# Kernel tuning notes

Measured on AMD Instinct MI355X. Metric: run time of the kernel, lower is better.

## Reference

```python
import jax, jax.numpy as jnp
import numpy as np

C = 256
HEADS = 4
GROUPS = 8
EPS = 1e-5


def setup_inputs() -> dict:
    key = jax.random.key(0)
    ks = jax.random.split(key, 7)
    B, H, W = 2, 64, 64
    x = jax.random.normal(ks[0], (B, C, H, W), dtype=jnp.float32)
    gamma = jnp.ones((C,), dtype=jnp.float32)
    beta = jnp.zeros((C,), dtype=jnp.float32)
    # conv 1x1 weights stored as [out_ch, in_ch]
    w_qkv = jax.random.normal(ks[1], (3 * C, C), dtype=jnp.float32) * (1.0 / np.sqrt(C))
    b_qkv = jax.random.normal(ks[2], (3 * C,), dtype=jnp.float32) * 0.01
    w_proj = jax.random.normal(ks[3], (C, C), dtype=jnp.float32) * (1.0 / np.sqrt(C))
    b_proj = jax.random.normal(ks[4], (C,), dtype=jnp.float32) * 0.01
    return {"x": x, "gamma": gamma, "beta": beta, "w_qkv": w_qkv,
            "b_qkv": b_qkv, "w_proj": w_proj, "b_proj": b_proj}


def _group_norm(x, gamma, beta):
    B, Cc, H, W = x.shape
    xg = x.reshape(B, GROUPS, Cc // GROUPS, H, W)
    mean = xg.mean(axis=(2, 3, 4), keepdims=True)
    var = xg.var(axis=(2, 3, 4), keepdims=True)
    xg = (xg - mean) * jax.lax.rsqrt(var + EPS)
    xn = xg.reshape(B, Cc, H, W)
    return xn * gamma[None, :, None, None] + beta[None, :, None, None]


def reference(x, gamma, beta, w_qkv, b_qkv, w_proj, b_proj):
    B, Cc, H, W = x.shape
    N = H * W
    hd = Cc // HEADS
    residual = x
    xn = _group_norm(x, gamma, beta)
    # 1x1 conv == channel matmul: [B,3C,H,W]
    qkv = jnp.einsum('oc,bchw->bohw', w_qkv, xn) + b_qkv[None, :, None, None]
    # [B,3,heads,hd,N] -> (3,B,heads,N,hd)
    qkv = qkv.reshape(B, 3, HEADS, hd, N).transpose(1, 0, 2, 4, 3)
    q, k, v = qkv[0], qkv[1], qkv[2]
    scale = hd ** -0.5
    attn = jax.nn.softmax(jnp.einsum('bhnd,bhmd->bhnm', q, k) * scale, axis=-1)
    out = jnp.einsum('bhnm,bhmd->bhnd', attn, v)  # [B,heads,N,hd]
    out = out.transpose(0, 1, 3, 2).reshape(B, Cc, H, W)
    out = jnp.einsum('oc,bchw->bohw', w_proj, out) + b_proj[None, :, None, None]
    return out + residual
```

## Files before the change

### kernel.cpp

```cpp
#include <hip/hip_runtime.h>
#include <stdint.h>

#define EPS 1e-5f

typedef float f32x4 __attribute__((ext_vector_type(4)));
typedef float f32x16 __attribute__((ext_vector_type(16)));
typedef __bf16 bf16x8 __attribute__((ext_vector_type(8)));
typedef uint32_t u32x4 __attribute__((ext_vector_type(4)));

__device__ __forceinline__ ushort f2bf(float f){
  union { float f; uint32_t u; } v; v.f = f;
  uint32_t r = v.u + 0x7fffu + ((v.u >> 16) & 1u);
  return (ushort)(r >> 16);
}

__device__ __forceinline__ float bf2f(ushort u){
  union { uint32_t u; float f; } v; v.u = ((uint32_t)u) << 16;
  return v.f;
}

__device__ __forceinline__ uint32_t pk2bf(float a, float b){
  __bf16 x = (__bf16)a, y = (__bf16)b;
  return (uint32_t)__builtin_bit_cast(ushort, x) |
         ((uint32_t)__builtin_bit_cast(ushort, y) << 16);
}

__device__ __forceinline__ f32x4 mfma16(bf16x8 a, bf16x8 b, f32x4 c){
  return __builtin_amdgcn_mfma_f32_16x16x32_bf16(a, b, c, 0, 0, 0);
}
__device__ __forceinline__ f32x16 mfma32(bf16x8 a, bf16x8 b, f32x16 c){
  return __builtin_amdgcn_mfma_f32_32x32x16_bf16(a, b, c, 0, 0, 0);
}

__global__ __launch_bounds__(256) void k_pg(const float* wq, const float* wp, const float* x,
                                            ushort* wqb, ushort* wpb, float2* part){
  __shared__ float red[8];
  int bid = blockIdx.x;
  if (bid < 768){
    int i = bid * 256 + threadIdx.x;
    if (i < 3*256*256) wqb[i] = f2bf(wq[i]);
    if (i < 256*256)   wpb[i] = f2bf(wp[i]);
    return;
  }
  int gb = bid - 768;
  int bg = gb >> 6, pb = gb & 63;
  const f32x4* base = (const f32x4*)(x + (size_t)bg*131072 + (size_t)pb*2048);
  float s = 0.f, ss = 0.f;
  #pragma unroll
  for (int it = 0; it < 2; ++it){
    f32x4 v = base[threadIdx.x + it*256];
    #pragma unroll
    for (int j = 0; j < 4; ++j){ s += v[j]; ss += v[j]*v[j]; }
  }
  #pragma unroll
  for (int off = 1; off < 64; off <<= 1){
    s  += __shfl_xor(s,  off);
    ss += __shfl_xor(ss, off);
  }
  int wid = threadIdx.x >> 6;
  if ((threadIdx.x & 63) == 0){ red[wid] = s; red[4 + wid] = ss; }
  __syncthreads();
  if (threadIdx.x == 0){
    part[gb] = make_float2(red[0]+red[1]+red[2]+red[3],
                           red[4]+red[5]+red[6]+red[7]);
  }
}

__global__ __launch_bounds__(512) void k_nqkv(const float* x, const float* gamma, const float* beta,
                                              const float2* part, const ushort* wqb, const float* bqkv,
                                              ushort* Qb, ushort* Kb, ushort* Vb){
  __shared__ ushort A[32][264];
  __shared__ ushort Cl[32][136];
  __shared__ float2 st[8];
  int nt = blockIdx.x, b = blockIdx.y;
  int t = threadIdx.x, lane = t & 63, wid = t >> 6;

  {
    float2 p = part[(b*8 + wid)*64 + lane];
    float s = p.x, ss = p.y;
    #pragma unroll
    for (int off = 1; off < 64; off <<= 1){
      s  += __shfl_xor(s,  off);
      ss += __shfl_xor(ss, off);
    }
    if (lane == 0){
      const float inv = 1.f / 131072.f;
      float mean = s * inv;
      float var  = ss * inv - mean*mean;
      st[wid] = make_float2(mean, rsqrtf(var + EPS));
    }
  }
  __syncthreads();

  {
    int c = t >> 1, nh = t & 1;
    float2 s0 = st[c >> 5];
    float g  = gamma[c] * s0.y;
    float bt = beta[c] - s0.x * g;
    const float* xr = x + ((size_t)(b*256 + c))*4096 + nt*32 + nh*16;
    #pragma unroll
    for (int j4 = 0; j4 < 4; ++j4){
      f32x4 v = *(const f32x4*)(xr + j4*4);
      #pragma unroll
      for (int e = 0; e < 4; ++e) A[nh*16 + j4*4 + e][c] = f2bf(v[e]*g + bt);
    }
  }
  __syncthreads();

  int l15 = lane & 15, g4 = lane >> 4;
  f32x4 acc[6][2];
  #pragma unroll
  for (int of = 0; of < 6; ++of)
    #pragma unroll
    for (int mf = 0; mf < 2; ++mf) acc[of][mf] = (f32x4){0.f,0.f,0.f,0.f};

  #pragma unroll
  for (int ks = 0; ks < 8; ++ks){
    bf16x8 a0 = *(const bf16x8*)&A[l15][ks*32 + g4*8];
    bf16x8 a1 = *(const bf16x8*)&A[16 + l15][ks*32 + g4*8];
    #pragma unroll
    for (int of = 0; of < 6; ++of){
      int o = of*128 + wid*16 + l15;
      bf16x8 bw = *(const bf16x8*)(wqb + (size_t)o*256 + ks*32 + g4*8);
      acc[of][0] = mfma16(a0, bw, acc[of][0]);
      acc[of][1] = mfma16(a1, bw, acc[of][1]);
    }
  }

  #pragma unroll
  for (int of = 0; of < 6; ++of){
    __syncthreads();
    int o = of*128 + wid*16 + l15;
    float bias = bqkv[o];
    #pragma unroll
    for (int mf = 0; mf < 2; ++mf)
      #pragma unroll
      for (int r = 0; r < 4; ++r)
        Cl[mf*16 + g4*4 + r][wid*16 + l15] = f2bf(acc[of][mf][r] + bias);
    __syncthreads();
    if (of < 4){
      ushort* basep = (of < 2) ? Qb : Kb;
      int nl = t >> 4, oc = (t & 15) * 8;
      int h = (of & 1)*2 + (oc >> 6), d0 = oc & 63;
      ushort* dst = basep + (((size_t)(b*4 + h))*4096 + nt*32 + nl)*64 + d0;
      *(uint4*)dst = *(uint4*)&Cl[nl][oc];
    } else {
      int dl = t >> 2, nc = (t & 3) * 8;
      int h = (of - 4)*2 + (dl >> 6), d = dl & 63;
      uint32_t pk[4];
      #pragma unroll
      for (int j = 0; j < 4; ++j){
        uint32_t lo = Cl[nc + 2*j][dl], hiu = Cl[nc + 2*j + 1][dl];
        pk[j] = lo | (hiu << 16);
      }
      ushort* dst = Vb + (((size_t)(b*4 + h))*64 + d)*4096 + nt*32 + nc;
      *(uint4*)dst = make_uint4(pk[0], pk[1], pk[2], pk[3]);
    }
  }
}

template<int SPLIT>
__global__ __launch_bounds__(256, 2) void k_attn(const ushort* Qb, const ushort* Kb,
                                                 const ushort* Vb, ushort* Opart, float2* ML){
  const float SCL2 = 0.125f * 1.44269504f;
  const int per_xcd = 16 * SPLIT;
  int xb = (blockIdx.x & 7) * per_xcd + (blockIdx.x >> 3);
  int bh = xb / per_xcd;
  int within = xb % per_xcd;
  int sp = within >> 4, q4 = within & 15;
  int t = threadIdx.x, wid = t >> 6, l = t & 63, l31 = l & 31, hi = l >> 5;
  int qt = q4*4 + wid;

  const ushort* Qg = Qb + (size_t)bh*262144;
  const ushort* Kg = Kb + (size_t)bh*262144;
  const ushort* Vg = Vb + (size_t)bh*262144;

  bf16x8 qf[2][4];
  #pragma unroll
  for (int q2 = 0; q2 < 2; ++q2)
    #pragma unroll
    for (int dsub = 0; dsub < 4; ++dsub)
      qf[q2][dsub] = *(const bf16x8*)(Qg + (size_t)(qt*64 + q2*32 + l31)*64 + dsub*16 + hi*8);

  int rowp = (l31 & 19) | ((l31 & 4) << 1) | ((l31 & 8) >> 1);
  const ushort* Kbase = Kg + (size_t)rowp*64 + hi*8;
  const ushort* Vbase = Vg + (size_t)l31*4096 + hi*8;

  f32x16 o[2][2];
  #pragma unroll
  for (int dt = 0; dt < 2; ++dt)
    #pragma unroll
    for (int q2 = 0; q2 < 2; ++q2)
      #pragma unroll
      for (int r = 0; r < 16; ++r) o[dt][q2][r] = 0.f;
  float m_s[2] = {-INFINITY, -INFINITY};
  float l_s[2] = {0.f, 0.f};

  const int kbBeg = sp * (64 / SPLIT), kbEnd = kbBeg + 64 / SPLIT;
  for (int kb = kbBeg; kb < kbEnd; ++kb){
    bf16x8 kf[2][4];
    #pragma unroll
    for (int kt = 0; kt < 2; ++kt)
      #pragma unroll
      for (int dsub = 0; dsub < 4; ++dsub)
        kf[kt][dsub] = *(const bf16x8*)(Kbase + (size_t)(kb*64 + kt*32)*64 + dsub*16);

    f32x16 s[2][2];
    __builtin_amdgcn_s_setprio(1);
    #pragma unroll
    for (int kt = 0; kt < 2; ++kt)
      #pragma unroll
      for (int q2 = 0; q2 < 2; ++q2){
        f32x16 acc;
        #pragma unroll
        for (int r = 0; r < 16; ++r) acc[r] = 0.f;
        #pragma unroll
        for (int dsub = 0; dsub < 4; ++dsub)
          acc = mfma32(kf[kt][dsub], qf[q2][dsub], acc);
        s[kt][q2] = acc;
      }
    __builtin_amdgcn_s_setprio(0);

    float vm[2];
    #pragma unroll
    for (int q2 = 0; q2 < 2; ++q2){
      float v = s[0][q2][0];
      #pragma unroll
      for (int kt = 0; kt < 2; ++kt)
        #pragma unroll
        for (int r = 0; r < 16; ++r) v = fmaxf(v, s[kt][q2][r]);
      v = fmaxf(v, __shfl_xor(v, 32));
      vm[q2] = v * SCL2;
    }
    if (__any(fmaxf(vm[0] - m_s[0], vm[1] - m_s[1]) > 8.f)){
      #pragma unroll
      for (int q2 = 0; q2 < 2; ++q2){
        float mn = fmaxf(m_s[q2], vm[q2]);
        float a = __builtin_amdgcn_exp2f(m_s[q2] - mn);
        m_s[q2] = mn; l_s[q2] *= a;
        #pragma unroll
        for (int dt = 0; dt < 2; ++dt)
          #pragma unroll
          for (int r = 0; r < 16; ++r) o[dt][q2][r] *= a;
      }
    }
    #pragma unroll
    for (int q2 = 0; q2 < 2; ++q2){
      float r0 = 0.f, r1 = 0.f, r2 = 0.f, r3 = 0.f;
      #pragma unroll
      for (int kt = 0; kt < 2; ++kt)
        #pragma unroll
        for (int r = 0; r < 16; r += 4){
          float e0 = __builtin_amdgcn_exp2f(__builtin_fmaf(s[kt][q2][r+0], SCL2, -m_s[q2]));
          float e1 = __builtin_amdgcn_exp2f(__builtin_fmaf(s[kt][q2][r+1], SCL2, -m_s[q2]));
          float e2 = __builtin_amdgcn_exp2f(__builtin_fmaf(s[kt][q2][r+2], SCL2, -m_s[q2]));
          float e3 = __builtin_amdgcn_exp2f(__builtin_fmaf(s[kt][q2][r+3], SCL2, -m_s[q2]));
          s[kt][q2][r+0] = e0; s[kt][q2][r+1] = e1;
          s[kt][q2][r+2] = e2; s[kt][q2][r+3] = e3;
          r0 += e0; r1 += e1; r2 += e2; r3 += e3;
        }
      float rr = (r0 + r1) + (r2 + r3);
      rr += __shfl_xor(rr, 32);
      l_s[q2] += rr;
    }

    bf16x8 pf[2][2][2];
    #pragma unroll
    for (int kt = 0; kt < 2; ++kt)
      #pragma unroll
      for (int ks = 0; ks < 2; ++ks)
        #pragma unroll
        for (int q2 = 0; q2 < 2; ++q2){
          u32x4 w;
          #pragma unroll
          for (int c = 0; c < 4; ++c)
            w[c] = pk2bf(s[kt][q2][8*ks + 2*c], s[kt][q2][8*ks + 2*c + 1]);
          pf[kt][ks][q2] = __builtin_bit_cast(bf16x8, w);
        }

    bf16x8 vf[2][4];
    #pragma unroll
    for (int dt = 0; dt < 2; ++dt)
      #pragma unroll
      for (int c4 = 0; c4 < 4; ++c4)
        vf[dt][c4] = *(const bf16x8*)(Vbase + (size_t)dt*131072 + kb*64 + c4*16);

    __builtin_amdgcn_s_setprio(1);
    #pragma unroll
    for (int dt = 0; dt < 2; ++dt)
      #pragma unroll
      for (int q2 = 0; q2 < 2; ++q2)
        #pragma unroll
        for (int kt = 0; kt < 2; ++kt)
          #pragma unroll
          for (int ks = 0; ks < 2; ++ks)
            o[dt][q2] = mfma32(vf[dt][kt*2 + ks], pf[kt][ks][q2], o[dt][q2]);
    __builtin_amdgcn_s_setprio(0);
  }

  int pw = (bh*SPLIT + sp)*64 + qt;
  if (hi == 0){
    ML[(size_t)pw*64 + l31]      = make_float2(m_s[0], l_s[0]);
    ML[(size_t)pw*64 + 32 + l31] = make_float2(m_s[1], l_s[1]);
  }
  ushort* dst = Opart + (size_t)pw*4096;
  #pragma unroll
  for (int q2 = 0; q2 < 2; ++q2){
    int nl = q2*32 + l31;
    #pragma unroll
    for (int dt = 0; dt < 2; ++dt)
      #pragma unroll
      for (int rq = 0; rq < 4; ++rq){
        int d0 = dt*32 + rq*8 + 4*hi;
        uint2 w = make_uint2(pk2bf(o[dt][q2][rq*4+0], o[dt][q2][rq*4+1]),
                             pk2bf(o[dt][q2][rq*4+2], o[dt][q2][rq*4+3]));
        *(uint2*)(dst + (size_t)nl*64 + d0) = w;
      }
  }
}

template<int SPLIT>
__global__ __launch_bounds__(256) void k_comb(const ushort* Opart, const float2* ML, ushort* AO){
  int qt = blockIdx.x, bh = blockIdx.y;
  int b = bh >> 2, h = bh & 3;
  int t = threadIdx.x, ql = t >> 2, d0 = (t & 3) * 16;

  float2 mls[SPLIT];
  float m = -INFINITY;
  #pragma unroll
  for (int sp = 0; sp < SPLIT; ++sp){
    mls[sp] = ML[((size_t)((bh*SPLIT + sp)*64 + qt))*64 + ql];
    m = fmaxf(m, mls[sp].x);
  }
  float den = 0.f, w[SPLIT];
  #pragma unroll
  for (int sp = 0; sp < SPLIT; ++sp){
    w[sp] = __builtin_amdgcn_exp2f(mls[sp].x - m);
    den += mls[sp].y * w[sp];
  }
  float inv = 1.f / den;

  float vals[16];
  #pragma unroll
  for (int j = 0; j < 16; ++j) vals[j] = 0.f;
  #pragma unroll
  for (int sp = 0; sp < SPLIT; ++sp){
    const ushort* src = Opart + ((size_t)((bh*SPLIT + sp)*64 + qt))*4096 + (size_t)ql*64 + d0;
    uint4 a0 = *(const uint4*)src;
    uint4 a1 = *(const uint4*)(src + 8);
    float f = w[sp] * inv;
    #pragma unroll
    for (int j = 0; j < 8; ++j) vals[j]   += bf2f(((const ushort*)&a0)[j]) * f;
    #pragma unroll
    for (int j = 0; j < 8; ++j) vals[j+8] += bf2f(((const ushort*)&a1)[j]) * f;
  }
  uint32_t pk[8];
  #pragma unroll
  for (int j = 0; j < 8; ++j) pk[j] = pk2bf(vals[2*j], vals[2*j+1]);
  ushort* dst = AO + ((size_t)b*4096 + qt*64 + ql)*256 + h*64 + d0;
  *(uint4*)dst       = make_uint4(pk[0], pk[1], pk[2], pk[3]);
  *(uint4*)(dst + 8) = make_uint4(pk[4], pk[5], pk[6], pk[7]);
}

__global__ __launch_bounds__(256) void k_proj(const ushort* AO, const ushort* wpb, const float* bproj,
                                              const float* x, float* out){
  int nt = blockIdx.x, ct = blockIdx.y, b = blockIdx.z;
  int t = threadIdx.x, lane = t & 63, wid = t >> 6, l15 = lane & 15, g4 = lane >> 4;
  int o = ct*64 + wid*16 + l15;
  f32x4 acc[4];
  #pragma unroll
  for (int m = 0; m < 4; ++m) acc[m] = (f32x4){0.f,0.f,0.f,0.f};

  #pragma unroll
  for (int ks = 0; ks < 8; ++ks){
    bf16x8 bw = *(const bf16x8*)(wpb + (size_t)o*256 + ks*32 + g4*8);
    #pragma unroll
    for (int mf = 0; mf < 4; ++mf){
      int n = nt*64 + mf*16 + l15;
      bf16x8 aa = *(const bf16x8*)(AO + ((size_t)b*4096 + n)*256 + ks*32 + g4*8);
      acc[mf] = mfma16(aa, bw, acc[mf]);
    }
  }

  float bias = bproj[o];
  size_t cbase = ((size_t)b*256 + o)*4096;
  #pragma unroll
  for (int mf = 0; mf < 4; ++mf){
    int n0 = nt*64 + mf*16 + g4*4;
    f32x4 res = *(const f32x4*)(x + cbase + n0);
    f32x4 ov;
    #pragma unroll
    for (int r = 0; r < 4; ++r) ov[r] = acc[mf][r] + bias + res[r];
    *(f32x4*)(out + cbase + n0) = ov;
  }
}

extern "C" void kernel_launch(void* const* d_in, const int* in_sizes, int n_in,
                              void* d_out, int out_size, void* d_ws, size_t ws_size,
                              hipStream_t stream) {
  const float* x     = (const float*)d_in[0];
  const float* gamma = (const float*)d_in[1];
  const float* beta  = (const float*)d_in[2];
  const float* wqkv  = (const float*)d_in[3];
  const float* bqkv  = (const float*)d_in[4];
  const float* wproj = (const float*)d_in[5];
  const float* bproj = (const float*)d_in[6];
  float* out = (float*)d_out;

  const size_t MiB = 1024*1024;
  char* ws = (char*)d_ws;
  float2* part   = (float2*)(ws + 0);
  ushort* wq_b   = (ushort*)(ws + 16384);
  ushort* wp_b   = (ushort*)(ws + 409600);
  ushort* Qb     = (ushort*)(ws + 1*MiB);
  ushort* Kb     = (ushort*)(ws + 5*MiB);
  ushort* Vb     = (ushort*)(ws + 9*MiB);
  ushort* AO     = (ushort*)(ws + 13*MiB);
  ushort* Opart  = (ushort*)(ws + 17*MiB);

  int split = (ws_size >= 35*MiB) ? 4 : (ws_size >= 26*MiB ? 2 : 1);
  float2* ML = (float2*)(ws + (17 + 4*(size_t)split)*MiB);

  k_pg  <<<1792, 256, 0, stream>>>(wqkv, wproj, x, wq_b, wp_b, part);
  k_nqkv<<<dim3(128,2), 512, 0, stream>>>(x, gamma, beta, part, wq_b, bqkv, Qb, Kb, Vb);
  if (split == 4){
    k_attn<4><<<512, 256, 0, stream>>>(Qb, Kb, Vb, Opart, ML);
    k_comb<4><<<dim3(64,8), 256, 0, stream>>>(Opart, ML, AO);
  } else if (split == 2){
    k_attn<2><<<256, 256, 0, stream>>>(Qb, Kb, Vb, Opart, ML);
    k_comb<2><<<dim3(64,8), 256, 0, stream>>>(Opart, ML, AO);
  } else {
    k_attn<1><<<128, 256, 0, stream>>>(Qb, Kb, Vb, Opart, ML);
    k_comb<1><<<dim3(64,8), 256, 0, stream>>>(Opart, ML, AO);
  }
  k_proj<<<dim3(64,4,2), 256, 0, stream>>>(AO, wp_b, bproj, x, out);
}
```

Measured before the change: 174.3 us.

## Shrink attention query tile per wave and fuse split-combine into projection

Each attention wave now handles 32 queries instead of 64. This halves the accumulator registers, lets the kernel request 4 blocks per CU, and doubles the grid. The V loads are issued before the QK MFMAs to overlap latency, and the XCD block swizzle is replaced with a plain bh-major mapping. The separate combine and projection kernels are merged into one kernel that combines the split partials into shared memory and then runs the output projection, so the AO round-trip and one launch go away. The trade-off is less reuse of each K/V load per wave, and the split=1 fallback is gone.

```diff
diff --git a/kernel.cpp b/kernel.cpp
--- a/kernel.cpp
+++ b/kernel.cpp
@@ -160,41 +160,34 @@
 }
 
 template<int SPLIT>
-__global__ __launch_bounds__(256, 2) void k_attn(const ushort* Qb, const ushort* Kb,
+__global__ __launch_bounds__(256, 4) void k_attn(const ushort* Qb, const ushort* Kb,
                                                  const ushort* Vb, ushort* Opart, float2* ML){
   const float SCL2 = 0.125f * 1.44269504f;
-  const int per_xcd = 16 * SPLIT;
-  int xb = (blockIdx.x & 7) * per_xcd + (blockIdx.x >> 3);
-  int bh = xb / per_xcd;
-  int within = xb % per_xcd;
-  int sp = within >> 4, q4 = within & 15;
+  int bh = blockIdx.x & 7;
+  int within = blockIdx.x >> 3;
+  int sp = within >> 5, qb = within & 31;
   int t = threadIdx.x, wid = t >> 6, l = t & 63, l31 = l & 31, hi = l >> 5;
-  int qt = q4*4 + wid;
+  int qt = qb*4 + wid;
 
   const ushort* Qg = Qb + (size_t)bh*262144;
   const ushort* Kg = Kb + (size_t)bh*262144;
   const ushort* Vg = Vb + (size_t)bh*262144;
 
-  bf16x8 qf[2][4];
-  #pragma unroll
-  for (int q2 = 0; q2 < 2; ++q2)
-    #pragma unroll
-    for (int dsub = 0; dsub < 4; ++dsub)
-      qf[q2][dsub] = *(const bf16x8*)(Qg + (size_t)(qt*64 + q2*32 + l31)*64 + dsub*16 + hi*8);
+  bf16x8 qf[4];
+  #pragma unroll
+  for (int dsub = 0; dsub < 4; ++dsub)
+    qf[dsub] = *(const bf16x8*)(Qg + (size_t)(qt*32 + l31)*64 + dsub*16 + hi*8);
 
   int rowp = (l31 & 19) | ((l31 & 4) << 1) | ((l31 & 8) >> 1);
   const ushort* Kbase = Kg + (size_t)rowp*64 + hi*8;
   const ushort* Vbase = Vg + (size_t)l31*4096 + hi*8;
 
-  f32x16 o[2][2];
+  f32x16 o[2];
   #pragma unroll
   for (int dt = 0; dt < 2; ++dt)
     #pragma unroll
-    for (int q2 = 0; q2 < 2; ++q2)
-      #pragma unroll
-      for (int r = 0; r < 16; ++r) o[dt][q2][r] = 0.f;
-  float m_s[2] = {-INFINITY, -INFINITY};
-  float l_s[2] = {0.f, 0.f};
+    for (int r = 0; r < 16; ++r) o[dt][r] = 0.f;
+  float m_s = -INFINITY, l_s = 0.f;
 
   const int kbBeg = sp * (64 / SPLIT), kbEnd = kbBeg + 64 / SPLIT;
   for (int kb = kbBeg; kb < kbEnd; ++kb){
@@ -205,193 +198,184 @@
       for (int dsub = 0; dsub < 4; ++dsub)
         kf[kt][dsub] = *(const bf16x8*)(Kbase + (size_t)(kb*64 + kt*32)*64 + dsub*16);
 
-    f32x16 s[2][2];
+    bf16x8 vf[2][4];
+    #pragma unroll
+    for (int dt = 0; dt < 2; ++dt)
+      #pragma unroll
+      for (int c4 = 0; c4 < 4; ++c4)
+        vf[dt][c4] = *(const bf16x8*)(Vbase + (size_t)dt*131072 + kb*64 + c4*16);
+
+    f32x16 s[2];
     __builtin_amdgcn_s_setprio(1);
     #pragma unroll
-    for (int kt = 0; kt < 2; ++kt)
-      #pragma unroll
-      for (int q2 = 0; q2 < 2; ++q2){
-        f32x16 acc;
+    for (int kt = 0; kt < 2; ++kt){
+      f32x16 acc;
+      #pragma unroll
+      for (int r = 0; r < 16; ++r) acc[r] = 0.f;
+      #pragma unroll
+      for (int dsub = 0; dsub < 4; ++dsub)
+        acc = mfma32(kf[kt][dsub], qf[dsub], acc);
+      s[kt] = acc;
+    }
+    __builtin_amdgcn_s_setprio(0);
+
+    f32x16 mx = s[0];
+    #pragma unroll
+    for (int r = 0; r < 16; ++r) mx[r] = fmaxf(mx[r], s[1][r]);
+    #pragma unroll
+    for (int off = 8; off > 0; off >>= 1)
+      #pragma unroll
+      for (int r = 0; r < off; ++r) mx[r] = fmaxf(mx[r], mx[r + off]);
+    float vm = fmaxf(mx[0], __shfl_xor(mx[0], 32)) * SCL2;
+
+    if (__any(vm > m_s + 8.f)){
+      float mn = fmaxf(m_s, vm);
+      float a = __builtin_amdgcn_exp2f(m_s - mn);
+      m_s = mn; l_s *= a;
+      #pragma unroll
+      for (int dt = 0; dt < 2; ++dt)
         #pragma unroll
-        for (int r = 0; r < 16; ++r) acc[r] = 0.f;
-        #pragma unroll
-        for (int dsub = 0; dsub < 4; ++dsub)
-          acc = mfma32(kf[kt][dsub], qf[q2][dsub], acc);
-        s[kt][q2] = acc;
-      }
-    __builtin_amdgcn_s_setprio(0);
-
-    float vm[2];
-    #pragma unroll
-    for (int q2 = 0; q2 < 2; ++q2){
-      float v = s[0][q2][0];
-      #pragma unroll
-      for (int kt = 0; kt < 2; ++kt)
-        #pragma unroll
-        for (int r = 0; r < 16; ++r) v = fmaxf(v, s[kt][q2][r]);
-      v = fmaxf(v, __shfl_xor(v, 32));
-      vm[q2] = v * SCL2;
-    }
-    if (__any(fmaxf(vm[0] - m_s[0], vm[1] - m_s[1]) > 8.f)){
-      #pragma unroll
-      for (int q2 = 0; q2 < 2; ++q2){
-        float mn = fmaxf(m_s[q2], vm[q2]);
-        float a = __builtin_amdgcn_exp2f(m_s[q2] - mn);
-        m_s[q2] = mn; l_s[q2] *= a;
-        #pragma unroll
-        for (int dt = 0; dt < 2; ++dt)
-          #pragma unroll
-          for (int r = 0; r < 16; ++r) o[dt][q2][r] *= a;
-      }
-    }
-    #pragma unroll
-    for (int q2 = 0; q2 < 2; ++q2){
+        for (int r = 0; r < 16; ++r) o[dt][r] *= a;
+    }
+    {
       float r0 = 0.f, r1 = 0.f, r2 = 0.f, r3 = 0.f;
       #pragma unroll
       for (int kt = 0; kt < 2; ++kt)
         #pragma unroll
         for (int r = 0; r < 16; r += 4){
-          float e0 = __builtin_amdgcn_exp2f(__builtin_fmaf(s[kt][q2][r+0], SCL2, -m_s[q2]));
-          float e1 = __builtin_amdgcn_exp2f(__builtin_fmaf(s[kt][q2][r+1], SCL2, -m_s[q2]));
-          float e2 = __builtin_amdgcn_exp2f(__builtin_fmaf(s[kt][q2][r+2], SCL2, -m_s[q2]));
-          float e3 = __builtin_amdgcn_exp2f(__builtin_fmaf(s[kt][q2][r+3], SCL2, -m_s[q2]));
-          s[kt][q2][r+0] = e0; s[kt][q2][r+1] = e1;
-          s[kt][q2][r+2] = e2; s[kt][q2][r+3] = e3;
+          float e0 = __builtin_amdgcn_exp2f(__builtin_fmaf(s[kt][r+0], SCL2, -m_s));
+          float e1 = __builtin_amdgcn_exp2f(__builtin_fmaf(s[kt][r+1], SCL2, -m_s));
+          float e2 = __builtin_amdgcn_exp2f(__builtin_fmaf(s[kt][r+2], SCL2, -m_s));
+          float e3 = __builtin_amdgcn_exp2f(__builtin_fmaf(s[kt][r+3], SCL2, -m_s));
+          s[kt][r+0] = e0; s[kt][r+1] = e1;
+          s[kt][r+2] = e2; s[kt][r+3] = e3;
           r0 += e0; r1 += e1; r2 += e2; r3 += e3;
         }
       float rr = (r0 + r1) + (r2 + r3);
       rr += __shfl_xor(rr, 32);
-      l_s[q2] += rr;
-    }
-
-    bf16x8 pf[2][2][2];
+      l_s += rr;
+    }
+
+    bf16x8 pf[2][2];
     #pragma unroll
     for (int kt = 0; kt < 2; ++kt)
       #pragma unroll
-      for (int ks = 0; ks < 2; ++ks)
+      for (int ks = 0; ks < 2; ++ks){
+        u32x4 w;
         #pragma unroll
-        for (int q2 = 0; q2 < 2; ++q2){
-          u32x4 w;
-          #pragma unroll
-          for (int c = 0; c < 4; ++c)
-            w[c] = pk2bf(s[kt][q2][8*ks + 2*c], s[kt][q2][8*ks + 2*c + 1]);
-          pf[kt][ks][q2] = __builtin_bit_cast(bf16x8, w);
-        }
-
-    bf16x8 vf[2][4];
+        for (int c = 0; c < 4; ++c)
+          w[c] = pk2bf(s[kt][8*ks + 2*c], s[kt][8*ks + 2*c + 1]);
+        pf[kt][ks] = __builtin_bit_cast(bf16x8, w);
+      }
+
+    __builtin_amdgcn_s_setprio(1);
     #pragma unroll
     for (int dt = 0; dt < 2; ++dt)
       #pragma unroll
-      for (int c4 = 0; c4 < 4; ++c4)
-        vf[dt][c4] = *(const bf16x8*)(Vbase + (size_t)dt*131072 + kb*64 + c4*16);
-
-    __builtin_amdgcn_s_setprio(1);
-    #pragma unroll
-    for (int dt = 0; dt < 2; ++dt)
-      #pragma unroll
-      for (int q2 = 0; q2 < 2; ++q2)
+      for (int kt = 0; kt < 2; ++kt)
         #pragma unroll
-        for (int kt = 0; kt < 2; ++kt)
-          #pragma unroll
-          for (int ks = 0; ks < 2; ++ks)
-            o[dt][q2] = mfma32(vf[dt][kt*2 + ks], pf[kt][ks][q2], o[dt][q2]);
+        for (int ks = 0; ks < 2; ++ks)
+          o[dt] = mfma32(vf[dt][kt*2 + ks], pf[kt][ks], o[dt]);
     __builtin_amdgcn_s_setprio(0);
   }
 
-  int pw = (bh*SPLIT + sp)*64 + qt;
-  if (hi == 0){
-    ML[(size_t)pw*64 + l31]      = make_float2(m_s[0], l_s[0]);
-    ML[(size_t)pw*64 + 32 + l31] = make_float2(m_s[1], l_s[1]);
-  }
-  ushort* dst = Opart + (size_t)pw*4096;
-  #pragma unroll
-  for (int q2 = 0; q2 < 2; ++q2){
-    int nl = q2*32 + l31;
-    #pragma unroll
-    for (int dt = 0; dt < 2; ++dt)
-      #pragma unroll
-      for (int rq = 0; rq < 4; ++rq){
-        int d0 = dt*32 + rq*8 + 4*hi;
-        uint2 w = make_uint2(pk2bf(o[dt][q2][rq*4+0], o[dt][q2][rq*4+1]),
-                             pk2bf(o[dt][q2][rq*4+2], o[dt][q2][rq*4+3]));
-        *(uint2*)(dst + (size_t)nl*64 + d0) = w;
-      }
-  }
+  int pw = (bh*SPLIT + sp)*128 + qt;
+  if (hi == 0) ML[(size_t)pw*32 + l31] = make_float2(m_s, l_s);
+  ushort* dst = Opart + (size_t)pw*2048;
+  #pragma unroll
+  for (int dt = 0; dt < 2; ++dt)
+    #pragma unroll
+    for (int rq = 0; rq < 4; ++rq){
+      int d0 = dt*32 + rq*8 + 4*hi;
+      uint2 w = make_uint2(pk2bf(o[dt][rq*4+0], o[dt][rq*4+1]),
+                           pk2bf(o[dt][rq*4+2], o[dt][rq*4+3]));
+      *(uint2*)(dst + (size_t)l31*64 + d0) = w;
+    }
 }
 
 template<int SPLIT>
-__global__ __launch_bounds__(256) void k_comb(const ushort* Opart, const float2* ML, ushort* AO){
-  int qt = blockIdx.x, bh = blockIdx.y;
-  int b = bh >> 2, h = bh & 3;
-  int t = threadIdx.x, ql = t >> 2, d0 = (t & 3) * 16;
-
-  float2 mls[SPLIT];
-  float m = -INFINITY;
-  #pragma unroll
-  for (int sp = 0; sp < SPLIT; ++sp){
-    mls[sp] = ML[((size_t)((bh*SPLIT + sp)*64 + qt))*64 + ql];
-    m = fmaxf(m, mls[sp].x);
-  }
-  float den = 0.f, w[SPLIT];
-  #pragma unroll
-  for (int sp = 0; sp < SPLIT; ++sp){
-    w[sp] = __builtin_amdgcn_exp2f(mls[sp].x - m);
-    den += mls[sp].y * w[sp];
-  }
-  float inv = 1.f / den;
-
-  float vals[16];
-  #pragma unroll
-  for (int j = 0; j < 16; ++j) vals[j] = 0.f;
-  #pragma unroll
-  for (int sp = 0; sp < SPLIT; ++sp){
-    const ushort* src = Opart + ((size_t)((bh*SPLIT + sp)*64 + qt))*4096 + (size_t)ql*64 + d0;
-    uint4 a0 = *(const uint4*)src;
-    uint4 a1 = *(const uint4*)(src + 8);
-    float f = w[sp] * inv;
-    #pragma unroll
-    for (int j = 0; j < 8; ++j) vals[j]   += bf2f(((const ushort*)&a0)[j]) * f;
-    #pragma unroll
-    for (int j = 0; j < 8; ++j) vals[j+8] += bf2f(((const ushort*)&a1)[j]) * f;
-  }
-  uint32_t pk[8];
-  #pragma unroll
-  for (int j = 0; j < 8; ++j) pk[j] = pk2bf(vals[2*j], vals[2*j+1]);
-  ushort* dst = AO + ((size_t)b*4096 + qt*64 + ql)*256 + h*64 + d0;
-  *(uint4*)dst       = make_uint4(pk[0], pk[1], pk[2], pk[3]);
-  *(uint4*)(dst + 8) = make_uint4(pk[4], pk[5], pk[6], pk[7]);
-}
-
-__global__ __launch_bounds__(256) void k_proj(const ushort* AO, const ushort* wpb, const float* bproj,
-                                              const float* x, float* out){
-  int nt = blockIdx.x, ct = blockIdx.y, b = blockIdx.z;
-  int t = threadIdx.x, lane = t & 63, wid = t >> 6, l15 = lane & 15, g4 = lane >> 4;
-  int o = ct*64 + wid*16 + l15;
-  f32x4 acc[4];
-  #pragma unroll
-  for (int m = 0; m < 4; ++m) acc[m] = (f32x4){0.f,0.f,0.f,0.f};
+__global__ __launch_bounds__(512) void k_cproj(const ushort* Opart, const float2* ML,
+                                               const ushort* wpb, const float* bproj,
+                                               const float* x, float* out){
+  __shared__ ushort A[64][264];
+  int nt = blockIdx.x, b = blockIdx.y;
+  int t = threadIdx.x;
+
+  int n_local = t >> 3, d0 = (t & 7) * 8;
+  int tile = n_local >> 5, ql = n_local & 31;
+  int qt32 = nt*2 + tile;
+  #pragma unroll
+  for (int h = 0; h < 4; ++h){
+    int bh = b*4 + h;
+    float2 mls[SPLIT];
+    float m = -INFINITY;
+    #pragma unroll
+    for (int sp = 0; sp < SPLIT; ++sp){
+      mls[sp] = ML[((size_t)((bh*SPLIT + sp)*128 + qt32))*32 + ql];
+      m = fmaxf(m, mls[sp].x);
+    }
+    float den = 0.f, w[SPLIT];
+    #pragma unroll
+    for (int sp = 0; sp < SPLIT; ++sp){
+      w[sp] = __builtin_amdgcn_exp2f(mls[sp].x - m);
+      den += mls[sp].y * w[sp];
+    }
+    float inv = 1.f / den;
+    float vals[8];
+    #pragma unroll
+    for (int j = 0; j < 8; ++j) vals[j] = 0.f;
+    #pragma unroll
+    for (int sp = 0; sp < SPLIT; ++sp){
+      const ushort* src = Opart + ((size_t)((bh*SPLIT + sp)*128 + qt32))*2048 + (size_t)ql*64 + d0;
+      uint4 a0 = *(const uint4*)src;
+      float f = w[sp] * inv;
+      #pragma unroll
+      for (int j = 0; j < 8; ++j) vals[j] += bf2f(((const ushort*)&a0)[j]) * f;
+    }
+    uint32_t pk[4];
+    #pragma unroll
+    for (int j = 0; j < 4; ++j) pk[j] = pk2bf(vals[2*j], vals[2*j+1]);
+    *(uint4*)&A[n_local][h*64 + d0] = make_uint4(pk[0], pk[1], pk[2], pk[3]);
+  }
+  __syncthreads();
+
+  int lane = t & 63, wid = t >> 6, l15 = lane & 15, g4 = lane >> 4;
+  f32x4 acc[4][2];
+  #pragma unroll
+  for (int mf = 0; mf < 4; ++mf)
+    #pragma unroll
+    for (int of = 0; of < 2; ++of) acc[mf][of] = (f32x4){0.f,0.f,0.f,0.f};
 
   #pragma unroll
   for (int ks = 0; ks < 8; ++ks){
-    bf16x8 bw = *(const bf16x8*)(wpb + (size_t)o*256 + ks*32 + g4*8);
+    bf16x8 aa[4];
+    #pragma unroll
+    for (int mf = 0; mf < 4; ++mf)
+      aa[mf] = *(const bf16x8*)&A[mf*16 + l15][ks*32 + g4*8];
+    #pragma unroll
+    for (int of = 0; of < 2; ++of){
+      int o = of*128 + wid*16 + l15;
+      bf16x8 bw = *(const bf16x8*)(wpb + (size_t)o*256 + ks*32 + g4*8);
+      #pragma unroll
+      for (int mf = 0; mf < 4; ++mf)
+        acc[mf][of] = mfma16(aa[mf], bw, acc[mf][of]);
+    }
+  }
+
+  #pragma unroll
+  for (int of = 0; of < 2; ++of){
+    int o = of*128 + wid*16 + l15;
+    float bias = bproj[o];
+    size_t cbase = ((size_t)b*256 + o)*4096;
     #pragma unroll
     for (int mf = 0; mf < 4; ++mf){
-      int n = nt*64 + mf*16 + l15;
-      bf16x8 aa = *(const bf16x8*)(AO + ((size_t)b*4096 + n)*256 + ks*32 + g4*8);
-      acc[mf] = mfma16(aa, bw, acc[mf]);
-    }
-  }
-
-  float bias = bproj[o];
-  size_t cbase = ((size_t)b*256 + o)*4096;
-  #pragma unroll
-  for (int mf = 0; mf < 4; ++mf){
-    int n0 = nt*64 + mf*16 + g4*4;
-    f32x4 res = *(const f32x4*)(x + cbase + n0);
-    f32x4 ov;
-    #pragma unroll
-    for (int r = 0; r < 4; ++r) ov[r] = acc[mf][r] + bias + res[r];
-    *(f32x4*)(out + cbase + n0) = ov;
+      int n0 = nt*64 + mf*16 + g4*4;
+      f32x4 res = *(const f32x4*)(x + cbase + n0);
+      f32x4 ov;
+      #pragma unroll
+      for (int r = 0; r < 4; ++r) ov[r] = acc[mf][of][r] + bias + res[r];
+      *(f32x4*)(out + cbase + n0) = ov;
+    }
   }
 }
 
@@ -415,23 +399,18 @@
   ushort* Qb     = (ushort*)(ws + 1*MiB);
   ushort* Kb     = (ushort*)(ws + 5*MiB);
   ushort* Vb     = (ushort*)(ws + 9*MiB);
-  ushort* AO     = (ushort*)(ws + 13*MiB);
-  ushort* Opart  = (ushort*)(ws + 17*MiB);
-
-  int split = (ws_size >= 35*MiB) ? 4 : (ws_size >= 26*MiB ? 2 : 1);
-  float2* ML = (float2*)(ws + (17 + 4*(size_t)split)*MiB);
+  ushort* Opart  = (ushort*)(ws + 13*MiB);
+
+  int split = (ws_size >= 31*MiB) ? 4 : 2;
+  float2* ML = (float2*)(ws + (13 + 4*(size_t)split)*MiB);
 
   k_pg  <<<1792, 256, 0, stream>>>(wqkv, wproj, x, wq_b, wp_b, part);
   k_nqkv<<<dim3(128,2), 512, 0, stream>>>(x, gamma, beta, part, wq_b, bqkv, Qb, Kb, Vb);
   if (split == 4){
-    k_attn<4><<<512, 256, 0, stream>>>(Qb, Kb, Vb, Opart, ML);
-    k_comb<4><<<dim3(64,8), 256, 0, stream>>>(Opart, ML, AO);
-  } else if (split == 2){
-    k_attn<2><<<256, 256, 0, stream>>>(Qb, Kb, Vb, Opart, ML);
-    k_comb<2><<<dim3(64,8), 256, 0, stream>>>(Opart, ML, AO);
+    k_attn<4><<<1024, 256, 0, stream>>>(Qb, Kb, Vb, Opart, ML);
+    k_cproj<4><<<dim3(64,2), 512, 0, stream>>>(Opart, ML, wp_b, bproj, x, out);
   } else {
-    k_attn<1><<<128, 256, 0, stream>>>(Qb, Kb, Vb, Opart, ML);
-    k_comb<1><<<dim3(64,8), 256, 0, stream>>>(Opart, ML, AO);
-  }
-  k_proj<<<dim3(64,4,2), 256, 0, stream>>>(AO, wp_b, bproj, x, out);
-}
+    k_attn<2><<<512, 256, 0, stream>>>(Qb, Kb, Vb, Opart, ML);
+    k_cproj<2><<<dim3(64,2), 512, 0, stream>>>(Opart, ML, wp_b, bproj, x, out);
+  }
+}
```

After: 261.2 us. 49.8% more time.
